# Performance work log

Measured on AMD Instinct MI355X. Metric: run time of the kernel, lower is better.

Reference implementation:

```python
import jax, jax.numpy as jnp
import numpy as np

N, E, G, D = 100000, 400000, 4000, 128
AF, BF, L = 74, 12, 11  # atom/bond feat sizes; L = n_layers-1 GNN layers after GetContext


def _p(k, shape, fan):
    return jax.random.normal(k, shape, dtype=jnp.float32) * (fan ** -0.5)


def setup_inputs() -> dict:
    key = jax.random.key(0)
    ks = iter(jax.random.split(key, 32))
    z = lambda *s: jnp.zeros(s, jnp.float32)
    return dict(
        atom_feats=jax.random.normal(next(ks), (N, AF), jnp.float32),
        bond_feats=jax.random.normal(next(ks), (E, BF), jnp.float32),
        src=jax.random.randint(next(ks), (E,), 0, N, jnp.int32),
        dst=jax.random.randint(next(ks), (E,), 0, N, jnp.int32),
        node_graph_ids=jnp.sort(jax.random.randint(next(ks), (N,), 0, G, jnp.int32)),
        W_node=_p(next(ks), (AF, D), AF), b_node=z(D),
        W_edge1=_p(next(ks), (AF + BF, D), AF + BF), b_edge1=z(D),
        W_edge2=_p(next(ks), (2 * D, 1), 2 * D), b_edge2=z(1),
        W_et=_p(next(ks), (D, D), D), b_et=z(D),
        gru0_Wih=_p(next(ks), (3 * D, D), D), gru0_bih=z(3 * D),
        gru0_Whh=_p(next(ks), (3 * D, D), D), gru0_bhh=z(3 * D),
        Wpe=_p(next(ks), (L, 2 * D, 1), 2 * D), bpe=z(L, 1),
        Wpn=_p(next(ks), (L, D, D), D), bpn=z(L, D),
        gru_Wih=_p(next(ks), (L, 3 * D, D), D), gru_bih=z(L, 3 * D),
        gru_Whh=_p(next(ks), (L, 3 * D, D), D), gru_bhh=z(L, 3 * D),
        Wr1=_p(next(ks), (D, D), D), br1=z(D),
        Wr2=_p(next(ks), (D, D), D), br2=z(D),
    )


def leaky_relu(x):
    return jnp.where(x > 0, x, 0.01 * x)


def edge_softmax(logits, dst):
    # softmax of edge logits grouped by destination node (DGL edge_softmax)
    m = jax.ops.segment_max(logits, dst, num_segments=N)
    m = jnp.where(jnp.isfinite(m), m, 0.0)
    e = jnp.exp(logits - m[dst])
    s = jax.ops.segment_sum(e, dst, num_segments=N)
    return e / s[dst]


def gru_cell(x, h, Wih, bih, Whh, bhh):
    gi = x @ Wih.T + bih
    gh = h @ Whh.T + bhh
    ir, iz, ig = jnp.split(gi, 3, axis=-1)
    hr, hz, hg = jnp.split(gh, 3, axis=-1)
    r = jax.nn.sigmoid(ir + hr)
    z = jax.nn.sigmoid(iz + hz)
    n = jnp.tanh(ig + r * hg)
    return (1.0 - z) * n + z * h


def _attentive_fp(atom_feats, bond_feats, src, dst, node_graph_ids,
                  W_node, b_node, W_edge1, b_edge1, W_edge2, b_edge2,
                  W_et, b_et, gru0_Wih, gru0_bih, gru0_Whh, gru0_bhh,
                  Wpe, bpe, Wpn, bpn, gru_Wih, gru_bih, gru_Whh, gru_bhh,
                  Wr1, br1, Wr2, br2):
    # --- GetContext (dropout = identity at inference) ---
    hv_new = leaky_relu(atom_feats @ W_node + b_node)                       # [N,D]
    he1 = leaky_relu(jnp.concatenate([atom_feats[src], bond_feats], 1) @ W_edge1 + b_edge1)  # [E,D]
    logits = leaky_relu(jnp.concatenate([hv_new[dst], he1], 1) @ W_edge2 + b_edge2)          # [E,1]
    a = edge_softmax(logits, dst)
    c = jax.ops.segment_sum(a * (he1 @ W_et + b_et), dst, num_segments=N)   # [N,D]
    h = jax.nn.relu(gru_cell(jax.nn.elu(c), hv_new, gru0_Wih, gru0_bih, gru0_Whh, gru0_bhh))

    # --- 11 GNNLayers (AttentiveGRU2) via scan over stacked params ---
    def layer(h, p):
        Wpe_l, bpe_l, Wpn_l, bpn_l, Wih, bih, Whh, bhh = p
        lg = leaky_relu(jnp.concatenate([h[dst], h[src]], 1) @ Wpe_l + bpe_l)  # [E,1]
        a = edge_softmax(lg, dst)
        hp = h @ Wpn_l + bpn_l
        c = jax.ops.segment_sum(hp[src] * a, dst, num_segments=N)
        return jax.nn.relu(gru_cell(jax.nn.elu(c), h, Wih, bih, Whh, bhh)), None

    h, _ = jax.lax.scan(layer, h, (Wpe, bpe, Wpn, bpn, gru_Wih, gru_bih, gru_Whh, gru_bhh))

    # --- MLPNodeReadout, mode='mean' ---
    x = jax.nn.relu(h @ Wr1 + br1) @ Wr2 + br2
    sums = jax.ops.segment_sum(x, node_graph_ids, num_segments=G)
    counts = jax.ops.segment_sum(jnp.ones((N, 1), x.dtype), node_graph_ids, num_segments=G)
    return sums / jnp.maximum(counts, 1.0)                                  # [G,D]


def reference(atom_feats, bond_feats, src, dst, node_graph_ids,
              W_node, b_node, W_edge1, b_edge1, W_edge2, b_edge2,
              W_et, b_et, gru0_Wih, gru0_bih, gru0_Whh, gru0_bhh,
              Wpe, bpe, Wpn, bpn, gru_Wih, gru_bih, gru_Whh, gru_bhh,
              Wr1, br1, Wr2, br2):
    return _attentive_fp(atom_feats, bond_feats, src, dst, node_graph_ids,
                         W_node, b_node, W_edge1, b_edge1, W_edge2, b_edge2,
                         W_et, b_et, gru0_Wih, gru0_bih, gru0_Whh, gru0_bhh,
                         Wpe, bpe, Wpn, bpn, gru_Wih, gru_bih, gru_Whh, gru_bhh,
                         Wr1, br1, Wr2, br2)
```

## Files before the change

kernel.cpp:

```cpp
#include <hip/hip_runtime.h>
#include <cstdio>
#include <cstddef>

enum { ACT_NONE = 0, ACT_LEAKY = 1, ACT_RELU = 2 };

typedef __attribute__((ext_vector_type(8))) short short8v;
typedef __attribute__((ext_vector_type(4))) float f32x4;

__device__ __forceinline__ float leakyf(float x) { return x > 0.f ? x : 0.01f * x; }

__device__ __forceinline__ unsigned fenc(float f) {
    unsigned u = __float_as_uint(f);
    return (u & 0x80000000u) ? ~u : (u | 0x80000000u);
}
__device__ __forceinline__ float fdec(unsigned u) {
    return (u & 0x80000000u) ? __uint_as_float(u & 0x7FFFFFFFu) : __uint_as_float(~u);
}

__device__ __forceinline__ unsigned bf16rtn(float x) {
    unsigned u = __float_as_uint(x);
    return (u + 0x7FFFu + ((u >> 16) & 1u)) >> 16;
}
__device__ __forceinline__ void split8(float4 a, float4 b, short8v& hi, short8v& lo) {
    const float v[8] = {a.x, a.y, a.z, a.w, b.x, b.y, b.z, b.w};
#pragma unroll
    for (int i = 0; i < 8; i++) {
        const unsigned hb = bf16rtn(v[i]);
        const float r = v[i] - __uint_as_float(hb << 16);
        hi[i] = (short)hb;
        lo[i] = (short)bf16rtn(r);
    }
}

__global__ __launch_bounds__(256) void wsplit_all_k(
    const float* __restrict__ g0_Wih, const float* __restrict__ g0_Whh,
    const float* __restrict__ gWih,   const float* __restrict__ gWhh,
    const float* __restrict__ Wpn,    const float* __restrict__ W_et,
    const float* __restrict__ Wr1,    const float* __restrict__ Wr2,
    const float* __restrict__ W_e1,   const float* __restrict__ W_node,
    unsigned short* __restrict__ gwHi, unsigned short* __restrict__ gwLo,
    unsigned short* __restrict__ wtHi, unsigned short* __restrict__ wtLo,
    unsigned short* __restrict__ w96Hi, unsigned short* __restrict__ w96Lo)
{
    const int b = blockIdx.x, t = threadIdx.x;
    if (b < 1152) {
        const int slot = b / 96, inner = b % 96;
        const int i4 = (inner * 256 + t) * 4;
        if (i4 >= 98304) return;
        const float* Wih = slot == 0 ? g0_Wih : gWih + (size_t)(slot - 1) * 49152;
        const float* Whh = slot == 0 ? g0_Whh : gWhh + (size_t)(slot - 1) * 49152;
        const float* src = (i4 < 49152) ? (Wih + i4) : (Whh + (i4 - 49152));
        const float4 v = *(const float4*)src;
        const float vv[4] = {v.x, v.y, v.z, v.w};
        unsigned short h4[4], l4[4];
#pragma unroll
        for (int i = 0; i < 4; i++) {
            const unsigned hb = bf16rtn(vv[i]);
            const float r = vv[i] - __uint_as_float(hb << 16);
            h4[i] = (unsigned short)hb;
            l4[i] = (unsigned short)bf16rtn(r);
        }
        *(ushort4*)&gwHi[(size_t)slot * 98304 + i4] = make_ushort4(h4[0], h4[1], h4[2], h4[3]);
        *(ushort4*)&gwLo[(size_t)slot * 98304 + i4] = make_ushort4(l4[0], l4[1], l4[2], l4[3]);
    } else if (b < 2048) {
        const int q = b - 1152;
        const int slot = q / 64, inner = q % 64;
        const int idx = inner * 256 + t;
        if (idx >= 16384) return;
        const float* W = slot < 11 ? Wpn + (size_t)slot * 16384
                        : slot == 11 ? W_et : slot == 12 ? Wr1 : Wr2;
        const int k = idx >> 7, col = idx & 127;
        const float v = W[idx];
        const unsigned hb = bf16rtn(v);
        const float r = v - __uint_as_float(hb << 16);
        wtHi[(size_t)slot * 16384 + col * 128 + k] = (unsigned short)hb;
        wtLo[(size_t)slot * 16384 + col * 128 + k] = (unsigned short)bf16rtn(r);
    } else {
        const int q = b - 2048;
        const int slot = q / 48, inner = q % 48;
        const int idx = inner * 256 + t;
        if (idx >= 12288) return;
        const float* W = slot == 0 ? W_e1 : W_node;
        const int K   = slot == 0 ? 86 : 74;
        const int col = idx / 96, k = idx - col * 96;
        const float v = (k < K) ? W[(size_t)k * 128 + col] : 0.f;
        const unsigned hb = bf16rtn(v);
        const float r = v - __uint_as_float(hb << 16);
        w96Hi[(size_t)slot * 12288 + idx] = (unsigned short)hb;
        w96Lo[(size_t)slot * 12288 + idx] = (unsigned short)bf16rtn(r);
    }
}

__global__ __launch_bounds__(512) void gru_fused_mfma_k(
    const float* __restrict__ cbuf, const unsigned short* __restrict__ whi,
    const unsigned short* __restrict__ wlo, const float* __restrict__ bih,
    const float* __restrict__ bhh, float* __restrict__ h,
    const float* __restrict__ wa, const float* __restrict__ wb,
    float* __restrict__ pd, float* __restrict__ ps,
    const unsigned short* __restrict__ w3hi, const unsigned short* __restrict__ w3lo,
    const float* __restrict__ b3, float* __restrict__ out3, int act3, int M)
{
    __shared__ __align__(16) char smem[64 * 132 * 4];
    short (*lhi)[4][64][8] = (short(*)[4][64][8])smem;
    short (*llo)[4][64][8] = (short(*)[4][64][8])(smem + 16384);
    float (*fbuf)[132] = (float(*)[132])smem;

    const int t    = threadIdx.x;
    const int lane = t & 63;
    const int w    = t >> 6;
    const int rBase = blockIdx.x * 64;

    const int sRS = t >> 3, sQ = t & 7;
    const int sRow = rBase + sRS;
    const int sRT = sRS >> 4, sLrow = sRS & 15;

    auto stage = [&](const float* __restrict__ A, bool doElu) {
#pragma unroll
        for (int half = 0; half < 2; half++) {
            const int k0 = sQ * 16 + half * 8;
            const int kc = k0 >> 5;
            const int g  = (k0 & 31) >> 3;
            float4 f0 = make_float4(0.f, 0.f, 0.f, 0.f);
            float4 f1 = make_float4(0.f, 0.f, 0.f, 0.f);
            if (sRow < M) {
                f0 = *(const float4*)&A[(size_t)sRow * 128 + k0];
                f1 = *(const float4*)&A[(size_t)sRow * 128 + k0 + 4];
                if (doElu) {
                    f0.x = f0.x > 0.f ? f0.x : expm1f(f0.x);
                    f0.y = f0.y > 0.f ? f0.y : expm1f(f0.y);
                    f0.z = f0.z > 0.f ? f0.z : expm1f(f0.z);
                    f0.w = f0.w > 0.f ? f0.w : expm1f(f0.w);
                    f1.x = f1.x > 0.f ? f1.x : expm1f(f1.x);
                    f1.y = f1.y > 0.f ? f1.y : expm1f(f1.y);
                    f1.z = f1.z > 0.f ? f1.z : expm1f(f1.z);
                    f1.w = f1.w > 0.f ? f1.w : expm1f(f1.w);
                }
            }
            short8v h8, l8;
            split8(f0, f1, h8, l8);
            *(short8v*)&lhi[sRT][kc][sLrow + g * 16][0] = h8;
            *(short8v*)&llo[sRT][kc][sLrow + g * 16][0] = l8;
        }
    };

    f32x4 accr[4], accz[4], accig[4], acchg[4];
#pragma unroll
    for (int rt = 0; rt < 4; rt++) {
        accr[rt]  = (f32x4){0.f, 0.f, 0.f, 0.f};
        accz[rt]  = (f32x4){0.f, 0.f, 0.f, 0.f};
        accig[rt] = (f32x4){0.f, 0.f, 0.f, 0.f};
        acchg[rt] = (f32x4){0.f, 0.f, 0.f, 0.f};
    }

    const int cw   = w * 16 + (lane & 15);
    const int koff = (lane >> 4) * 8;

    stage(cbuf, true);
    __syncthreads();
#pragma unroll
    for (int kc = 0; kc < 4; kc++) {
        short8v bh[3], bl[3];
#pragma unroll
        for (int g = 0; g < 3; g++) {
            const size_t off = (size_t)(g * 128 + cw) * 128 + kc * 32 + koff;
            bh[g] = *(const short8v*)&whi[off];
            bl[g] = *(const short8v*)&wlo[off];
        }
#pragma unroll
        for (int rt = 0; rt < 4; rt++) {
            const short8v ah = *(const short8v*)&lhi[rt][kc][lane][0];
            const short8v al = *(const short8v*)&llo[rt][kc][lane][0];
            accr[rt]  = __builtin_amdgcn_mfma_f32_16x16x32_bf16(ah, bh[0], accr[rt], 0, 0, 0);
            accr[rt]  = __builtin_amdgcn_mfma_f32_16x16x32_bf16(al, bh[0], accr[rt], 0, 0, 0);
            accr[rt]  = __builtin_amdgcn_mfma_f32_16x16x32_bf16(ah, bl[0], accr[rt], 0, 0, 0);
            accz[rt]  = __builtin_amdgcn_mfma_f32_16x16x32_bf16(ah, bh[1], accz[rt], 0, 0, 0);
            accz[rt]  = __builtin_amdgcn_mfma_f32_16x16x32_bf16(al, bh[1], accz[rt], 0, 0, 0);
            accz[rt]  = __builtin_amdgcn_mfma_f32_16x16x32_bf16(ah, bl[1], accz[rt], 0, 0, 0);
            accig[rt] = __builtin_amdgcn_mfma_f32_16x16x32_bf16(ah, bh[2], accig[rt], 0, 0, 0);
            accig[rt] = __builtin_amdgcn_mfma_f32_16x16x32_bf16(al, bh[2], accig[rt], 0, 0, 0);
            accig[rt] = __builtin_amdgcn_mfma_f32_16x16x32_bf16(ah, bl[2], accig[rt], 0, 0, 0);
        }
    }
    __syncthreads();

    stage(h, false);
    __syncthreads();
#pragma unroll
    for (int kc = 0; kc < 4; kc++) {
        short8v bh[3], bl[3];
#pragma unroll
        for (int g = 0; g < 3; g++) {
            const size_t off = (size_t)(384 + g * 128 + cw) * 128 + kc * 32 + koff;
            bh[g] = *(const short8v*)&whi[off];
            bl[g] = *(const short8v*)&wlo[off];
        }
#pragma unroll
        for (int rt = 0; rt < 4; rt++) {
            const short8v ah = *(const short8v*)&lhi[rt][kc][lane][0];
            const short8v al = *(const short8v*)&llo[rt][kc][lane][0];
            accr[rt]  = __builtin_amdgcn_mfma_f32_16x16x32_bf16(ah, bh[0], accr[rt], 0, 0, 0);
            accr[rt]  = __builtin_amdgcn_mfma_f32_16x16x32_bf16(al, bh[0], accr[rt], 0, 0, 0);
            accr[rt]  = __builtin_amdgcn_mfma_f32_16x16x32_bf16(ah, bl[0], accr[rt], 0, 0, 0);
            accz[rt]  = __builtin_amdgcn_mfma_f32_16x16x32_bf16(ah, bh[1], accz[rt], 0, 0, 0);
            accz[rt]  = __builtin_amdgcn_mfma_f32_16x16x32_bf16(al, bh[1], accz[rt], 0, 0, 0);
            accz[rt]  = __builtin_amdgcn_mfma_f32_16x16x32_bf16(ah, bl[1], accz[rt], 0, 0, 0);
            acchg[rt] = __builtin_amdgcn_mfma_f32_16x16x32_bf16(ah, bh[2], acchg[rt], 0, 0, 0);
            acchg[rt] = __builtin_amdgcn_mfma_f32_16x16x32_bf16(al, bh[2], acchg[rt], 0, 0, 0);
            acchg[rt] = __builtin_amdgcn_mfma_f32_16x16x32_bf16(ah, bl[2], acchg[rt], 0, 0, 0);
        }
    }

    const bool post = (wa != nullptr) || (w3hi != nullptr);
    const float br_  = bih[cw] + bhh[cw];
    const float bz_  = bih[128 + cw] + bhh[128 + cw];
    const float big_ = bih[256 + cw];
    const float bhg_ = bhh[256 + cw];
    if (post) __syncthreads();
#pragma unroll
    for (int rt = 0; rt < 4; rt++) {
        const int lr0 = rt * 16 + ((lane >> 4) << 2);
#pragma unroll
        for (int i = 0; i < 4; i++) {
            const int row = rBase + lr0 + i;
            const bool ok = (row < M);
            float hnew = 0.f;
            if (ok) {
                const float hv = h[(size_t)row * 128 + cw];
                const float r  = 1.f / (1.f + expf(-(accr[rt][i] + br_)));
                const float z  = 1.f / (1.f + expf(-(accz[rt][i] + bz_)));
                const float nn = tanhf(accig[rt][i] + big_ + r * (acchg[rt][i] + bhg_));
                hnew = fmaxf((1.f - z) * nn + z * hv, 0.f);
                h[(size_t)row * 128 + cw] = hnew;
            }
            if (post) fbuf[lr0 + i][cw] = hnew;
        }
    }
    if (!post) return;
    __syncthreads();

    if (wa && t < 64 && rBase + t < M) {
        float accd = 0.f, accs = 0.f;
        for (int cc = 0; cc < 128; cc++) {
            const float hv = fbuf[t][cc];
            accd = fmaf(hv, wa[cc], accd);
            accs = fmaf(hv, wb[cc], accs);
        }
        pd[rBase + t] = accd;
        ps[rBase + t] = accs;
    }

    if (w3hi) {
        float4 rv[2][2];
#pragma unroll
        for (int half = 0; half < 2; half++) {
            const int k0 = sQ * 16 + half * 8;
            rv[half][0] = *(const float4*)&fbuf[sRS][k0];
            rv[half][1] = *(const float4*)&fbuf[sRS][k0 + 4];
        }
        __syncthreads();
#pragma unroll
        for (int half = 0; half < 2; half++) {
            const int k0 = sQ * 16 + half * 8;
            const int kc = k0 >> 5;
            const int g  = (k0 & 31) >> 3;
            short8v h8, l8;
            split8(rv[half][0], rv[half][1], h8, l8);
            *(short8v*)&lhi[sRT][kc][sLrow + g * 16][0] = h8;
            *(short8v*)&llo[sRT][kc][sLrow + g * 16][0] = l8;
        }
        __syncthreads();

        f32x4 acc3[4];
#pragma unroll
        for (int rt = 0; rt < 4; rt++) acc3[rt] = (f32x4){0.f, 0.f, 0.f, 0.f};
#pragma unroll
        for (int kc = 0; kc < 4; kc++) {
            const size_t off = (size_t)cw * 128 + kc * 32 + koff;
            const short8v bh = *(const short8v*)&w3hi[off];
            const short8v bl = *(const short8v*)&w3lo[off];
#pragma unroll
            for (int rt = 0; rt < 4; rt++) {
                const short8v ah = *(const short8v*)&lhi[rt][kc][lane][0];
                const short8v al = *(const short8v*)&llo[rt][kc][lane][0];
                acc3[rt] = __builtin_amdgcn_mfma_f32_16x16x32_bf16(ah, bh, acc3[rt], 0, 0, 0);
                acc3[rt] = __builtin_amdgcn_mfma_f32_16x16x32_bf16(al, bh, acc3[rt], 0, 0, 0);
                acc3[rt] = __builtin_amdgcn_mfma_f32_16x16x32_bf16(ah, bl, acc3[rt], 0, 0, 0);
            }
        }
        const float b0 = b3[cw];
#pragma unroll
        for (int rt = 0; rt < 4; rt++) {
            const int r0 = rBase + rt * 16 + ((lane >> 4) << 2);
#pragma unroll
            for (int i = 0; i < 4; i++) {
                const int row = r0 + i;
                if (row >= M) continue;
                float v = acc3[rt][i] + b0;
                if (act3 == ACT_LEAKY)      v = v > 0.f ? v : 0.01f * v;
                else if (act3 == ACT_RELU)  v = fmaxf(v, 0.f);
                out3[(size_t)row * 128 + cw] = v;
            }
        }
    }
}

__global__ __launch_bounds__(512) void mfma128_k(
    const float* __restrict__ A, const unsigned short* __restrict__ whi,
    const unsigned short* __restrict__ wlo, const float* __restrict__ bias,
    float* __restrict__ C, int M, int actOut)
{
    __shared__ short lhi[4][4][64][8];
    __shared__ short llo[4][4][64][8];
    const int t    = threadIdx.x;
    const int lane = t & 63;
    const int w    = t >> 6;
    const int rBase = blockIdx.x * 64;

    {
        const int rS = t >> 3, q = t & 7;
        const int row = rBase + rS;
        const int rt = rS >> 4, lrow = rS & 15;
#pragma unroll
        for (int half = 0; half < 2; half++) {
            const int k0 = q * 16 + half * 8;
            const int kc = k0 >> 5;
            const int g  = (k0 & 31) >> 3;
            float4 f0 = make_float4(0.f, 0.f, 0.f, 0.f);
            float4 f1 = make_float4(0.f, 0.f, 0.f, 0.f);
            if (row < M) {
                f0 = *(const float4*)&A[(size_t)row * 128 + k0];
                f1 = *(const float4*)&A[(size_t)row * 128 + k0 + 4];
            }
            short8v h8, l8;
            split8(f0, f1, h8, l8);
            *(short8v*)&lhi[rt][kc][lrow + g * 16][0] = h8;
            *(short8v*)&llo[rt][kc][lrow + g * 16][0] = l8;
        }
    }
    __syncthreads();

    f32x4 acc[4];
#pragma unroll
    for (int rt = 0; rt < 4; rt++) acc[rt] = (f32x4){0.f, 0.f, 0.f, 0.f};

    const int cw   = w * 16 + (lane & 15);
    const int koff = (lane >> 4) * 8;

#pragma unroll
    for (int kc = 0; kc < 4; kc++) {
        const size_t off = (size_t)cw * 128 + kc * 32 + koff;
        const short8v bh = *(const short8v*)&whi[off];
        const short8v bl = *(const short8v*)&wlo[off];
#pragma unroll
        for (int rt = 0; rt < 4; rt++) {
            const short8v ah = *(const short8v*)&lhi[rt][kc][lane][0];
            const short8v al = *(const short8v*)&llo[rt][kc][lane][0];
            acc[rt] = __builtin_amdgcn_mfma_f32_16x16x32_bf16(ah, bh, acc[rt], 0, 0, 0);
            acc[rt] = __builtin_amdgcn_mfma_f32_16x16x32_bf16(al, bh, acc[rt], 0, 0, 0);
            acc[rt] = __builtin_amdgcn_mfma_f32_16x16x32_bf16(ah, bl, acc[rt], 0, 0, 0);
        }
    }

    const float b0 = bias[cw];
#pragma unroll
    for (int rt = 0; rt < 4; rt++) {
        const int r0 = rBase + rt * 16 + ((lane >> 4) << 2);
#pragma unroll
        for (int i = 0; i < 4; i++) {
            const int row = r0 + i;
            if (row >= M) continue;
            float v = acc[rt][i] + b0;
            if (actOut == ACT_LEAKY)      v = v > 0.f ? v : 0.01f * v;
            else if (actOut == ACT_RELU)  v = fmaxf(v, 0.f);
            C[(size_t)row * 128 + cw] = v;
        }
    }
}

__global__ __launch_bounds__(512) void mfma96_k(
    const float* __restrict__ A1, const float* __restrict__ A2,
    const int* __restrict__ idx,
    const unsigned short* __restrict__ whi, const unsigned short* __restrict__ wlo,
    const float* __restrict__ bias, float* __restrict__ C,
    const float* __restrict__ dotW, float* __restrict__ dotOut,
    const float* __restrict__ ee, const float* __restrict__ sd,
    const int* __restrict__ dstI, float* __restrict__ cAtom,
    int writeC, int M, int K1, int actOut)
{
    __shared__ __align__(16) char smem[64 * 130 * 4];
    short (*lhi)[3][64][8] = (short(*)[3][64][8])smem;
    short (*llo)[3][64][8] = (short(*)[3][64][8])(smem + 12288);
    float (*fbuf)[130] = (float(*)[130])smem;

    const int t    = threadIdx.x;
    const int lane = t & 63;
    const int w    = t >> 6;
    const int rBase = blockIdx.x * 64;

    {
        const int rS = t >> 3, q = t & 7;
        const int row = rBase + rS;
        const int rt = rS >> 4, lrow = rS & 15;
#pragma unroll
        for (int half = 0; half < 2; half++) {
            const int k0 = q * 16 + half * 8;
            if (k0 >= 96) continue;
            const int kc = k0 >> 5;
            const int g  = (k0 & 31) >> 3;
            float v[8] = {0.f, 0.f, 0.f, 0.f, 0.f, 0.f, 0.f, 0.f};
            if (row < M) {
                const int ar = idx ? idx[row] : row;
                const float* __restrict__ a1 = A1 + (size_t)ar * K1;
#pragma unroll
                for (int j = 0; j < 8; j++) {
                    const int k = k0 + j;
                    if (k < K1)                 v[j] = a1[k];
                    else if (A2 && k < K1 + 12) v[j] = A2[(size_t)row * 12 + (k - K1)];
                }
            }
            short8v h8, l8;
            split8(make_float4(v[0], v[1], v[2], v[3]),
                   make_float4(v[4], v[5], v[6], v[7]), h8, l8);
            *(short8v*)&lhi[rt][kc][lrow + g * 16][0] = h8;
            *(short8v*)&llo[rt][kc][lrow + g * 16][0] = l8;
        }
    }
    __syncthreads();

    f32x4 acc[4];
#pragma unroll
    for (int rt = 0; rt < 4; rt++) acc[rt] = (f32x4){0.f, 0.f, 0.f, 0.f};

    const int cw   = w * 16 + (lane & 15);
    const int koff = (lane >> 4) * 8;

#pragma unroll
    for (int kc = 0; kc < 3; kc++) {
        const size_t off = (size_t)cw * 96 + kc * 32 + koff;
        const short8v bh = *(const short8v*)&whi[off];
        const short8v bl = *(const short8v*)&wlo[off];
#pragma unroll
        for (int rt = 0; rt < 4; rt++) {
            const short8v ah = *(const short8v*)&lhi[rt][kc][lane][0];
            const short8v al = *(const short8v*)&llo[rt][kc][lane][0];
            acc[rt] = __builtin_amdgcn_mfma_f32_16x16x32_bf16(ah, bh, acc[rt], 0, 0, 0);
            acc[rt] = __builtin_amdgcn_mfma_f32_16x16x32_bf16(al, bh, acc[rt], 0, 0, 0);
            acc[rt] = __builtin_amdgcn_mfma_f32_16x16x32_bf16(ah, bl, acc[rt], 0, 0, 0);
        }
    }

    const float b0 = bias[cw];
    if (dotOut) __syncthreads();
#pragma unroll
    for (int rt = 0; rt < 4; rt++) {
        const int lr0 = rt * 16 + ((lane >> 4) << 2);
#pragma unroll
        for (int i = 0; i < 4; i++) {
            const int row = rBase + lr0 + i;
            const bool ok = (row < M);
            float v = acc[rt][i] + b0;
            if (actOut == ACT_LEAKY)      v = v > 0.f ? v : 0.01f * v;
            else if (actOut == ACT_RELU)  v = fmaxf(v, 0.f);
            if (ok && writeC) C[(size_t)row * 128 + cw] = v;
            if (ok && ee) {
                const int d = dstI[row];
                const float a = ee[row] / sd[d];
                atomicAdd(&cAtom[(size_t)d * 128 + cw], a * v);
            }
            if (dotOut) fbuf[lr0 + i][cw] = ok ? v : 0.f;
        }
    }
    if (dotOut) {
        __syncthreads();
        if (t < 64 && rBase + t < M) {
            float accd = 0.f;
            for (int cc = 0; cc < 128; cc++)
                accd = fmaf(fbuf[t][cc], dotW[cc], accd);
            dotOut[rBase + t] = accd;
        }
    }
}

__global__ __launch_bounds__(256) void edge_lgc_k(
    const float* __restrict__ pd, const float* __restrict__ pe,
    const float* __restrict__ b2, const int* __restrict__ dst,
    float* __restrict__ lg, unsigned* __restrict__ m_u, int E)
{
    const int e = blockIdx.x * blockDim.x + threadIdx.x;
    if (e >= E) return;
    const int d = dst[e];
    const float v = leakyf(pd[d] + pe[e] + b2[0]);
    lg[e] = v;
    atomicMax(&m_u[d], fenc(v));
}

__global__ __launch_bounds__(256) void edge_exp_k(
    float* __restrict__ lg, const unsigned* __restrict__ m_u,
    float* __restrict__ s, const int* __restrict__ dst, int E)
{
    const int e = blockIdx.x * blockDim.x + threadIdx.x;
    if (e >= E) return;
    const int d = dst[e];
    const float ex = expf(lg[e] - fdec(m_u[d]));
    lg[e] = ex;
    atomicAdd(&s[d], ex);
}

__global__ __launch_bounds__(256) void hist_k(
    const int* __restrict__ dst, unsigned* __restrict__ cnt, int E)
{
    const int e = blockIdx.x * blockDim.x + threadIdx.x;
    if (e < E) atomicAdd(&cnt[dst[e]], 1u);
}

__global__ __launch_bounds__(1024) void scan_k(
    const unsigned* __restrict__ cnt, int* __restrict__ rp, int N)
{
    __shared__ int wsum[16];
    __shared__ int carry;
    const int t = threadIdx.x, lane = t & 63, wid = t >> 6;
    if (t == 0) carry = 0;
    __syncthreads();
    for (int base = 0; base < N; base += 1024) {
        const int i = base + t;
        const int v = (i < N) ? (int)cnt[i] : 0;
        int x = v;
#pragma unroll
        for (int o = 1; o < 64; o <<= 1) {
            const int y = __shfl_up(x, o, 64);
            if (lane >= o) x += y;
        }
        if (lane == 63) wsum[wid] = x;
        __syncthreads();
        if (wid == 0) {
            const int wv = (lane < 16) ? wsum[lane] : 0;
            int wx = wv;
#pragma unroll
            for (int o = 1; o < 16; o <<= 1) {
                const int y = __shfl_up(wx, o, 64);
                if (lane >= o) wx += y;
            }
            if (lane < 16) wsum[lane] = wx - wv;
        }
        __syncthreads();
        const int excl = carry + wsum[wid] + x - v;
        if (i < N) rp[i] = excl;
        __syncthreads();
        if (t == 1023) carry = excl + v;
        __syncthreads();
    }
    if (t == 0) rp[N] = carry;
}

__global__ __launch_bounds__(256) void fill_csr_k(
    const int* __restrict__ dst, int* __restrict__ pos,
    int* __restrict__ eidx, int E)
{
    const int e = blockIdx.x * blockDim.x + threadIdx.x;
    if (e < E) {
        const int p = atomicAdd(&pos[dst[e]], 1);
        eidx[p] = e;
    }
}

__global__ __launch_bounds__(256) void layer_gather_k(
    const int* __restrict__ rp, const int* __restrict__ eidx,
    const int* __restrict__ src,
    const float* __restrict__ pd, const float* __restrict__ ps,
    const float* __restrict__ bpe,
    const float* __restrict__ hp, float* __restrict__ c, int N)
{
    const int d = blockIdx.x * 4 + (threadIdx.x >> 6);
    const int l = threadIdx.x & 63;
    if (d >= N) return;
    const int beg = rp[d], end = rp[d + 1];
    float acc0 = 0.f, acc1 = 0.f;
    if (beg < end) {
        const float pdd = pd[d];
        const float b   = bpe[0];
        float m = -3.4e38f;
        for (int e = beg + l; e < end; e += 64)
            m = fmaxf(m, leakyf(pdd + ps[src[eidx[e]]] + b));
#pragma unroll
        for (int o = 32; o; o >>= 1) m = fmaxf(m, __shfl_xor(m, o, 64));
        float s = 0.f;
        for (int e = beg + l; e < end; e += 64)
            s += expf(leakyf(pdd + ps[src[eidx[e]]] + b) - m);
#pragma unroll
        for (int o = 32; o; o >>= 1) s += __shfl_xor(s, o, 64);
        const float inv = 1.f / s;
        for (int e = beg; e < end; ++e) {
            const int sr = src[eidx[e]];
            const float a = expf(leakyf(pdd + ps[sr] + b) - m) * inv;
            const float2 v = *(const float2*)&hp[(size_t)sr * 128 + l * 2];
            acc0 = fmaf(a, v.x, acc0);
            acc1 = fmaf(a, v.y, acc1);
        }
    }
    *(float2*)&c[(size_t)d * 128 + l * 2] = make_float2(acc0, acc1);
}

__global__ __launch_bounds__(256) void readout_mean_k(
    const float* __restrict__ x, const int* __restrict__ grp,
    float* __restrict__ out, int G)
{
    const int g = blockIdx.x * 4 + (threadIdx.x >> 6);
    const int l = threadIdx.x & 63;
    if (g >= G) return;
    const int beg = grp[g], end = grp[g + 1];
    float s0 = 0.f, s1 = 0.f;
    for (int r = beg; r < end; ++r) {
        const float2 v = *(const float2*)&x[(size_t)r * 128 + l * 2];
        s0 += v.x;
        s1 += v.y;
    }
    const float inv = 1.f / fmaxf((float)(end - beg), 1.f);
    *(float2*)&out[(size_t)g * 128 + l * 2] = make_float2(s0 * inv, s1 * inv);
}

extern "C" void kernel_launch(void* const* d_in, const int* in_sizes, int n_in,
                              void* d_out, int out_size, void* d_ws, size_t ws_size,
                              hipStream_t stream)
{
    const float* atom   = (const float*)d_in[0];
    const float* bond   = (const float*)d_in[1];
    const int*   src    = (const int*)d_in[2];
    const int*   dst    = (const int*)d_in[3];
    const int*   ngid   = (const int*)d_in[4];
    const float* W_node = (const float*)d_in[5];
    const float* b_node = (const float*)d_in[6];
    const float* W_e1   = (const float*)d_in[7];
    const float* b_e1   = (const float*)d_in[8];
    const float* W_e2   = (const float*)d_in[9];
    const float* b_e2   = (const float*)d_in[10];
    const float* W_et   = (const float*)d_in[11];
    const float* b_et   = (const float*)d_in[12];
    const float* g0_Wih = (const float*)d_in[13];
    const float* g0_bih = (const float*)d_in[14];
    const float* g0_Whh = (const float*)d_in[15];
    const float* g0_bhh = (const float*)d_in[16];
    const float* Wpe    = (const float*)d_in[17];
    const float* bpe    = (const float*)d_in[18];
    const float* Wpn    = (const float*)d_in[19];
    const float* bpn    = (const float*)d_in[20];
    const float* gWih   = (const float*)d_in[21];
    const float* gbih   = (const float*)d_in[22];
    const float* gWhh   = (const float*)d_in[23];
    const float* gbhh   = (const float*)d_in[24];
    const float* Wr1    = (const float*)d_in[25];
    const float* br1    = (const float*)d_in[26];
    const float* Wr2    = (const float*)d_in[27];
    const float* br2    = (const float*)d_in[28];

    const int N = in_sizes[0] / 74;
    const int E = in_sizes[1] / 12;
    const int G = out_size / 128;
    const int L = in_sizes[18];

    char* w = (char*)d_ws;
    auto align256 = [](size_t b) { return (b + 255) & ~(size_t)255; };
    auto alloc = [&](size_t bytes) {
        void* p = (void*)w;
        w += align256(bytes);
        return p;
    };
    float*    h    = (float*)alloc((size_t)N * 128 * 4);
    float*    c    = (float*)alloc((size_t)N * 128 * 4);
    float*    hp   = (float*)alloc((size_t)N * 128 * 4);
    int*      rp   = (int*)alloc((size_t)(N + 1) * 4);
    int*      posb = (int*)alloc((size_t)N * 4);
    int*      eidx = (int*)alloc((size_t)E * 4);
    int*      grp  = (int*)alloc((size_t)(G + 1) * 4);
    unsigned short* gwHi  = (unsigned short*)alloc((size_t)12 * 98304 * 2);
    unsigned short* gwLo  = (unsigned short*)alloc((size_t)12 * 98304 * 2);
    unsigned short* wtHi  = (unsigned short*)alloc((size_t)14 * 16384 * 2);
    unsigned short* wtLo  = (unsigned short*)alloc((size_t)14 * 16384 * 2);
    unsigned short* w96Hi = (unsigned short*)alloc((size_t)2 * 12288 * 2);
    unsigned short* w96Lo = (unsigned short*)alloc((size_t)2 * 12288 * 2);
    float*    pd   = (float*)alloc((size_t)N * 4);
    float*    ps   = (float*)alloc((size_t)N * 4);
    unsigned* m_u  = (unsigned*)alloc((size_t)N * 4);
    float*    sden = (float*)alloc((size_t)N * 4);
    float*    pe   = (float*)alloc((size_t)E * 4);
    float*    lg   = (float*)alloc((size_t)E * 4);
    if ((size_t)(w - (char*)d_ws) > ws_size) {
        fprintf(stderr, "kernel_launch: ws too small: need %zu, have %zu\n",
                (size_t)(w - (char*)d_ws), ws_size);
        return;
    }
    float* out = (float*)d_out;

    const dim3 blk(256);
    auto g64 = [](int M) { return dim3((unsigned)((M + 63) / 64)); };
    const dim3 gEdge((unsigned)((E + 255) / 256));

    wsplit_all_k<<<dim3(2144), blk, 0, stream>>>(
        g0_Wih, g0_Whh, gWih, gWhh, Wpn, W_et, Wr1, Wr2, W_e1, W_node,
        gwHi, gwLo, wtHi, wtLo, w96Hi, w96Lo);

    auto run_gru = [&](int slot, const float* bih, const float* bhh,
                       const float* wav, const float* wbv,
                       int w3slot, const float* b3, float* out3, int act3) {
        gru_fused_mfma_k<<<g64(N), dim3(512), 0, stream>>>(
            c, gwHi + (size_t)slot * 98304, gwLo + (size_t)slot * 98304,
            bih, bhh, h, wav, wbv, pd, ps,
            wtHi + (size_t)w3slot * 16384, wtLo + (size_t)w3slot * 16384,
            b3, out3, act3, N);
    };
    auto run_mfma128 = [&](const float* A, int slot, const float* bias,
                           float* C, int act) {
        mfma128_k<<<g64(N), dim3(512), 0, stream>>>(
            A, wtHi + (size_t)slot * 16384, wtLo + (size_t)slot * 16384, bias, C, N, act);
    };

    hipMemsetAsync(m_u, 0, (size_t)N * 4, stream);
    hist_k<<<gEdge, blk, 0, stream>>>(dst, m_u, E);
    scan_k<<<dim3(1), dim3(1024), 0, stream>>>(m_u, rp, N);
    hipMemcpyAsync(posb, rp, (size_t)N * 4, hipMemcpyDeviceToDevice, stream);
    fill_csr_k<<<gEdge, blk, 0, stream>>>(dst, posb, eidx, E);
    hipMemsetAsync(m_u, 0, (size_t)G * 4, stream);
    hist_k<<<dim3((unsigned)((N + 255) / 256)), blk, 0, stream>>>(ngid, m_u, N);
    scan_k<<<dim3(1), dim3(1024), 0, stream>>>(m_u, grp, G);

    mfma96_k<<<g64(N), dim3(512), 0, stream>>>(
        atom, nullptr, nullptr, w96Hi + 12288, w96Lo + 12288, b_node, h,
        W_e2, pd, nullptr, nullptr, nullptr, nullptr, 1, N, 74, ACT_LEAKY);
    mfma96_k<<<g64(E), dim3(512), 0, stream>>>(
        atom, bond, src, w96Hi, w96Lo, b_e1,
        nullptr, W_e2 + 128, pe, nullptr, nullptr, nullptr, nullptr, 0, E, 74, ACT_LEAKY);
    hipMemsetAsync(m_u, 0, (size_t)N * 4, stream);
    hipMemsetAsync(sden, 0, (size_t)N * 4, stream);
    edge_lgc_k<<<gEdge, blk, 0, stream>>>(pd, pe, b_e2, dst, lg, m_u, E);
    edge_exp_k<<<gEdge, blk, 0, stream>>>(lg, m_u, sden, dst, E);
    hipMemsetAsync(c, 0, (size_t)N * 128 * 4, stream);
    mfma96_k<<<g64(E), dim3(512), 0, stream>>>(
        atom, bond, src, w96Hi, w96Lo, b_e1,
        nullptr, nullptr, nullptr, lg, sden, dst, c, 0, E, 74, ACT_LEAKY);
    run_mfma128(c, 11, b_et, c, ACT_NONE);
    run_gru(0, g0_bih, g0_bhh, Wpe, Wpe + 128, 0, bpn, hp, ACT_NONE);

    for (int l = 0; l < L; ++l) {
        layer_gather_k<<<dim3((unsigned)((N + 3) / 4)), blk, 0, stream>>>(
            rp, eidx, src, pd, ps, bpe + l, hp, c, N);
        const bool more = (l + 1 < L);
        if (more) {
            run_gru(l + 1, gbih + (size_t)l * 384, gbhh + (size_t)l * 384,
                    Wpe + (size_t)(l + 1) * 256, Wpe + (size_t)(l + 1) * 256 + 128,
                    l + 1, bpn + (size_t)(l + 1) * 128, hp, ACT_NONE);
        } else {
            run_gru(l + 1, gbih + (size_t)l * 384, gbhh + (size_t)l * 384,
                    nullptr, nullptr, 12, br1, c, ACT_RELU);
        }
    }

    run_mfma128(c, 13, br2, hp, ACT_NONE);
    readout_mean_k<<<dim3((unsigned)((G + 3) / 4)), blk, 0, stream>>>(hp, grp, out, G);

    (void)n_in;
}
```

Baseline: 3.505 ms.

## Fuse per-layer attention gather into GRU kernel and sort edges by destination

```diff
diff --git a/kernel.cpp b/kernel.cpp
--- a/kernel.cpp
+++ b/kernel.cpp
@@ -31,6 +31,7 @@
         lo[i] = (short)bf16rtn(r);
     }
 }
+__device__ __forceinline__ float eluf(float x) { return x > 0.f ? x : expm1f(x); }
 
 __global__ __launch_bounds__(256) void wsplit_all_k(
     const float* __restrict__ g0_Wih, const float* __restrict__ g0_Whh,
@@ -98,7 +99,10 @@
     const float* __restrict__ wa, const float* __restrict__ wb,
     float* __restrict__ pd, float* __restrict__ ps,
     const unsigned short* __restrict__ w3hi, const unsigned short* __restrict__ w3lo,
-    const float* __restrict__ b3, float* __restrict__ out3, int act3, int M)
+    const float* __restrict__ b3, float* __restrict__ out3, int act3,
+    const int* __restrict__ grp_rp, const int* __restrict__ gsrc,
+    const float* __restrict__ ghp, const float* __restrict__ gbpe,
+    const float* __restrict__ pdIn, const float* __restrict__ psIn, int M)
 {
     __shared__ __align__(16) char smem[64 * 132 * 4];
     short (*lhi)[4][64][8] = (short(*)[4][64][8])smem;
@@ -126,14 +130,8 @@
                 f0 = *(const float4*)&A[(size_t)sRow * 128 + k0];
                 f1 = *(const float4*)&A[(size_t)sRow * 128 + k0 + 4];
                 if (doElu) {
-                    f0.x = f0.x > 0.f ? f0.x : expm1f(f0.x);
-                    f0.y = f0.y > 0.f ? f0.y : expm1f(f0.y);
-                    f0.z = f0.z > 0.f ? f0.z : expm1f(f0.z);
-                    f0.w = f0.w > 0.f ? f0.w : expm1f(f0.w);
-                    f1.x = f1.x > 0.f ? f1.x : expm1f(f1.x);
-                    f1.y = f1.y > 0.f ? f1.y : expm1f(f1.y);
-                    f1.z = f1.z > 0.f ? f1.z : expm1f(f1.z);
-                    f1.w = f1.w > 0.f ? f1.w : expm1f(f1.w);
+                    f0.x = eluf(f0.x); f0.y = eluf(f0.y); f0.z = eluf(f0.z); f0.w = eluf(f0.w);
+                    f1.x = eluf(f1.x); f1.y = eluf(f1.y); f1.z = eluf(f1.z); f1.w = eluf(f1.w);
                 }
             }
             short8v h8, l8;
@@ -155,8 +153,67 @@
     const int cw   = w * 16 + (lane & 15);
     const int koff = (lane >> 4) * 8;
 
-    stage(cbuf, true);
+    if (grp_rp) {
+        const float b = gbpe[0];
+#pragma unroll
+        for (int j = 0; j < 8; j++) {
+            const int lrow = w * 8 + j;
+            const int d = rBase + lrow;
+            float acc0 = 0.f, acc1 = 0.f;
+            if (d < M) {
+                const int beg = grp_rp[d], end = grp_rp[d + 1];
+                if (beg < end) {
+                    const float pdd = pdIn[d];
+                    float m = -3.4e38f;
+                    for (int e = beg + lane; e < end; e += 64)
+                        m = fmaxf(m, leakyf(pdd + psIn[gsrc[e]] + b));
+#pragma unroll
+                    for (int o = 32; o; o >>= 1) m = fmaxf(m, __shfl_xor(m, o, 64));
+                    float s = 0.f;
+                    for (int e = beg + lane; e < end; e += 64)
+                        s += expf(leakyf(pdd + psIn[gsrc[e]] + b) - m);
+#pragma unroll
+                    for (int o = 32; o; o >>= 1) s += __shfl_xor(s, o, 64);
+                    const float inv = 1.f / s;
+                    for (int e = beg; e < end; ++e) {
+                        const int sr = gsrc[e];
+                        const float a = expf(leakyf(pdd + psIn[sr] + b) - m) * inv;
+                        const float2 v = *(const float2*)&ghp[(size_t)sr * 128 + lane * 2];
+                        acc0 = fmaf(a, v.x, acc0);
+                        acc1 = fmaf(a, v.y, acc1);
+                    }
+                }
+            }
+            fbuf[lrow][lane * 2]     = acc0;
+            fbuf[lrow][lane * 2 + 1] = acc1;
+        }
+        __syncthreads();
+        float4 rv[2][2];
+#pragma unroll
+        for (int half = 0; half < 2; half++) {
+            const int k0 = sQ * 16 + half * 8;
+            rv[half][0] = *(const float4*)&fbuf[sRS][k0];
+            rv[half][1] = *(const float4*)&fbuf[sRS][k0 + 4];
+        }
+        __syncthreads();
+#pragma unroll
+        for (int half = 0; half < 2; half++) {
+            const int k0 = sQ * 16 + half * 8;
+            const int kc = k0 >> 5;
+            const int g  = (k0 & 31) >> 3;
+            float4 f0 = rv[half][0], f1 = rv[half][1];
+            f0.x = eluf(f0.x); f0.y = eluf(f0.y); f0.z = eluf(f0.z); f0.w = eluf(f0.w);
+            f1.x = eluf(f1.x); f1.y = eluf(f1.y); f1.z = eluf(f1.z); f1.w = eluf(f1.w);
+            short8v h8, l8;
+            split8(f0, f1, h8, l8);
+            *(short8v*)&lhi[sRT][kc][sLrow + g * 16][0] = h8;
+            *(short8v*)&llo[sRT][kc][sLrow + g * 16][0] = l8;
+        }
+    } else {
+        stage(cbuf, true);
+    }
     __syncthreads();
+
 #pragma unroll
     for (int kc = 0; kc < 4; kc++) {
         short8v bh[3], bl[3];
@@ -379,7 +436,7 @@
 
 __global__ __launch_bounds__(512) void mfma96_k(
     const float* __restrict__ A1, const float* __restrict__ A2,
-    const int* __restrict__ idx,
+    const int* __restrict__ idx, const int* __restrict__ idx2,
     const unsigned short* __restrict__ whi, const unsigned short* __restrict__ wlo,
     const float* __restrict__ bias, float* __restrict__ C,
     const float* __restrict__ dotW, float* __restrict__ dotOut,
@@ -409,13 +466,14 @@
             const int g  = (k0 & 31) >> 3;
             float v[8] = {0.f, 0.f, 0.f, 0.f, 0.f, 0.f, 0.f, 0.f};
             if (row < M) {
-                const int ar = idx ? idx[row] : row;
+                const int ar  = idx ? idx[row] : row;
+                const int ar2 = idx2 ? idx2[row] : row;
                 const float* __restrict__ a1 = A1 + (size_t)ar * K1;
 #pragma unroll
                 for (int j = 0; j < 8; j++) {
                     const int k = k0 + j;
                     if (k < K1)                 v[j] = a1[k];
-                    else if (A2 && k < K1 + 12) v[j] = A2[(size_t)row * 12 + (k - K1)];
+                    else if (A2 && k < K1 + 12) v[j] = A2[(size_t)ar2 * 12 + (k - K1)];
                 }
             }
             short8v h8, l8;
@@ -450,7 +508,8 @@
     }
 
     const float b0 = bias[cw];
-    if (dotOut) __syncthreads();
+    const bool useF = (dotOut != nullptr) || (ee != nullptr);
+    if (useF) __syncthreads();
 #pragma unroll
     for (int rt = 0; rt < 4; rt++) {
         const int lr0 = rt * 16 + ((lane >> 4) << 2);
@@ -462,15 +521,37 @@
             if (actOut == ACT_LEAKY)      v = v > 0.f ? v : 0.01f * v;
             else if (actOut == ACT_RELU)  v = fmaxf(v, 0.f);
             if (ok && writeC) C[(size_t)row * 128 + cw] = v;
-            if (ok && ee) {
-                const int d = dstI[row];
-                const float a = ee[row] / sd[d];
-                atomicAdd(&cAtom[(size_t)d * 128 + cw], a * v);
-            }
-            if (dotOut) fbuf[lr0 + i][cw] = ok ? v : 0.f;
-        }
-    }
-    if (dotOut) {
+            if (ee) {
+                float av = 0.f;
+                if (ok) {
+                    const int eo = idx2 ? idx2[row] : row;
+                    av = ee[eo] / sd[dstI[row]] * v;
+                }
+                fbuf[lr0 + i][cw] = av;
+            } else if (dotOut) {
+                fbuf[lr0 + i][cw] = ok ? v : 0.f;
+            }
+        }
+    }
+    if (ee) {
+        __syncthreads();
+        const int col = t & 127;
+        const int r0  = (t >> 7) * 16;
+        float acc2 = 0.f;
+        int cur = -1;
+        for (int j = 0; j < 16; j++) {
+            const int row = rBase + r0 + j;
+            if (row >= M) break;
+            const int d = dstI[row];
+            if (d != cur) {
+                if (cur >= 0) atomicAdd(&cAtom[(size_t)cur * 128 + col], acc2);
+                cur = d;
+                acc2 = 0.f;
+            }
+            acc2 += fbuf[r0 + j][col];
+        }
+        if (cur >= 0) atomicAdd(&cAtom[(size_t)cur * 128 + col], acc2);
+    } else if (dotOut) {
         __syncthreads();
         if (t < 64 && rBase + t < M) {
             float accd = 0.f;
@@ -553,51 +634,18 @@
 }
 
 __global__ __launch_bounds__(256) void fill_csr_k(
-    const int* __restrict__ dst, int* __restrict__ pos,
-    int* __restrict__ eidx, int E)
+    const int* __restrict__ dst, const int* __restrict__ src,
+    int* __restrict__ pos, int* __restrict__ eidx,
+    int* __restrict__ srcS, int* __restrict__ dstS, int E)
 {
     const int e = blockIdx.x * blockDim.x + threadIdx.x;
     if (e < E) {
-        const int p = atomicAdd(&pos[dst[e]], 1);
+        const int d = dst[e];
+        const int p = atomicAdd(&pos[d], 1);
         eidx[p] = e;
-    }
-}
-
-__global__ __launch_bounds__(256) void layer_gather_k(
-    const int* __restrict__ rp, const int* __restrict__ eidx,
-    const int* __restrict__ src,
-    const float* __restrict__ pd, const float* __restrict__ ps,
-    const float* __restrict__ bpe,
-    const float* __restrict__ hp, float* __restrict__ c, int N)
-{
-    const int d = blockIdx.x * 4 + (threadIdx.x >> 6);
-    const int l = threadIdx.x & 63;
-    if (d >= N) return;
-    const int beg = rp[d], end = rp[d + 1];
-    float acc0 = 0.f, acc1 = 0.f;
-    if (beg < end) {
-        const float pdd = pd[d];
-        const float b   = bpe[0];
-        float m = -3.4e38f;
-        for (int e = beg + l; e < end; e += 64)
-            m = fmaxf(m, leakyf(pdd + ps[src[eidx[e]]] + b));
-#pragma unroll
-        for (int o = 32; o; o >>= 1) m = fmaxf(m, __shfl_xor(m, o, 64));
-        float s = 0.f;
-        for (int e = beg + l; e < end; e += 64)
-            s += expf(leakyf(pdd + ps[src[eidx[e]]] + b) - m);
-#pragma unroll
-        for (int o = 32; o; o >>= 1) s += __shfl_xor(s, o, 64);
-        const float inv = 1.f / s;
-        for (int e = beg; e < end; ++e) {
-            const int sr = src[eidx[e]];
-            const float a = expf(leakyf(pdd + ps[sr] + b) - m) * inv;
-            const float2 v = *(const float2*)&hp[(size_t)sr * 128 + l * 2];
-            acc0 = fmaf(a, v.x, acc0);
-            acc1 = fmaf(a, v.y, acc1);
-        }
-    }
-    *(float2*)&c[(size_t)d * 128 + l * 2] = make_float2(acc0, acc1);
+        srcS[p] = src[e];
+        dstS[p] = d;
+    }
 }
 
 __global__ __launch_bounds__(256) void readout_mean_k(
@@ -666,10 +714,13 @@
     };
     float*    h    = (float*)alloc((size_t)N * 128 * 4);
     float*    c    = (float*)alloc((size_t)N * 128 * 4);
-    float*    hp   = (float*)alloc((size_t)N * 128 * 4);
+    float*    hpA  = (float*)alloc((size_t)N * 128 * 4);
+    float*    hpB  = (float*)alloc((size_t)N * 128 * 4);
     int*      rp   = (int*)alloc((size_t)(N + 1) * 4);
     int*      posb = (int*)alloc((size_t)N * 4);
     int*      eidx = (int*)alloc((size_t)E * 4);
+    int*      srcS = (int*)alloc((size_t)E * 4);
+    int*      dstS = (int*)alloc((size_t)E * 4);
     int*      grp  = (int*)alloc((size_t)(G + 1) * 4);
     unsigned short* gwHi  = (unsigned short*)alloc((size_t)12 * 98304 * 2);
     unsigned short* gwLo  = (unsigned short*)alloc((size_t)12 * 98304 * 2);
@@ -677,8 +728,10 @@
     unsigned short* wtLo  = (unsigned short*)alloc((size_t)14 * 16384 * 2);
     unsigned short* w96Hi = (unsigned short*)alloc((size_t)2 * 12288 * 2);
     unsigned short* w96Lo = (unsigned short*)alloc((size_t)2 * 12288 * 2);
-    float*    pd   = (float*)alloc((size_t)N * 4);
-    float*    ps   = (float*)alloc((size_t)N * 4);
+    float*    pdA  = (float*)alloc((size_t)N * 4);
+    float*    psA  = (float*)alloc((size_t)N * 4);
+    float*    pdB  = (float*)alloc((size_t)N * 4);
+    float*    psB  = (float*)alloc((size_t)N * 4);
     unsigned* m_u  = (unsigned*)alloc((size_t)N * 4);
     float*    sden = (float*)alloc((size_t)N * 4);
     float*    pe   = (float*)alloc((size_t)E * 4);
@@ -700,12 +753,16 @@
 
     auto run_gru = [&](int slot, const float* bih, const float* bhh,
                        const float* wav, const float* wbv,
-                       int w3slot, const float* b3, float* out3, int act3) {
+                       float* pdW, float* psW,
+                       int w3slot, const float* b3, float* out3, int act3,
+                       const float* gBpe, const float* hpR,
+                       const float* pdR, const float* psR) {
         gru_fused_mfma_k<<<g64(N), dim3(512), 0, stream>>>(
             c, gwHi + (size_t)slot * 98304, gwLo + (size_t)slot * 98304,
-            bih, bhh, h, wav, wbv, pd, ps,
+            bih, bhh, h, wav, wbv, pdW, psW,
             wtHi + (size_t)w3slot * 16384, wtLo + (size_t)w3slot * 16384,
-            b3, out3, act3, N);
+            b3, out3, act3,
+            gBpe ? rp : nullptr, srcS, hpR, gBpe, pdR, psR, N);
     };
     auto run_mfma128 = [&](const float* A, int slot, const float* bias,
                            float* C, int act) {
@@ -717,44 +774,53 @@
     hist_k<<<gEdge, blk, 0, stream>>>(dst, m_u, E);
     scan_k<<<dim3(1), dim3(1024), 0, stream>>>(m_u, rp, N);
     hipMemcpyAsync(posb, rp, (size_t)N * 4, hipMemcpyDeviceToDevice, stream);
-    fill_csr_k<<<gEdge, blk, 0, stream>>>(dst, posb, eidx, E);
+    fill_csr_k<<<gEdge, blk, 0, stream>>>(dst, src, posb, eidx, srcS, dstS, E);
     hipMemsetAsync(m_u, 0, (size_t)G * 4, stream);
     hist_k<<<dim3((unsigned)((N + 255) / 256)), blk, 0, stream>>>(ngid, m_u, N);
     scan_k<<<dim3(1), dim3(1024), 0, stream>>>(m_u, grp, G);
 
     mfma96_k<<<g64(N), dim3(512), 0, stream>>>(
-        atom, nullptr, nullptr, w96Hi + 12288, w96Lo + 12288, b_node, h,
-        W_e2, pd, nullptr, nullptr, nullptr, nullptr, 1, N, 74, ACT_LEAKY);
+        atom, nullptr, nullptr, nullptr, w96Hi + 12288, w96Lo + 12288, b_node, h,
+        W_e2, pdA, nullptr, nullptr, nullptr, nullptr, 1, N, 74, ACT_LEAKY);
     mfma96_k<<<g64(E), dim3(512), 0, stream>>>(
-        atom, bond, src, w96Hi, w96Lo, b_e1,
+        atom, bond, src, nullptr, w96Hi, w96Lo, b_e1,
         nullptr, W_e2 + 128, pe, nullptr, nullptr, nullptr, nullptr, 0, E, 74, ACT_LEAKY);
     hipMemsetAsync(m_u, 0, (size_t)N * 4, stream);
     hipMemsetAsync(sden, 0, (size_t)N * 4, stream);
-    edge_lgc_k<<<gEdge, blk, 0, stream>>>(pd, pe, b_e2, dst, lg, m_u, E);
+    edge_lgc_k<<<gEdge, blk, 0, stream>>>(pdA, pe, b_e2, dst, lg, m_u, E);
     edge_exp_k<<<gEdge, blk, 0, stream>>>(lg, m_u, sden, dst, E);
     hipMemsetAsync(c, 0, (size_t)N * 128 * 4, stream);
     mfma96_k<<<g64(E), dim3(512), 0, stream>>>(
-        atom, bond, src, w96Hi, w96Lo, b_e1,
-        nullptr, nullptr, nullptr, lg, sden, dst, c, 0, E, 74, ACT_LEAKY);
+        atom, bond, srcS, eidx, w96Hi, w96Lo, b_e1,
+        nullptr, nullptr, nullptr, lg, sden, dstS, c, 0, E, 74, ACT_LEAKY);
     run_mfma128(c, 11, b_et, c, ACT_NONE);
-    run_gru(0, g0_bih, g0_bhh, Wpe, Wpe + 128, 0, bpn, hp, ACT_NONE);
+    run_gru(0, g0_bih, g0_bhh, Wpe, Wpe + 128, pdA, psA,
+            0, bpn, hpA, ACT_NONE, nullptr, nullptr, nullptr, nullptr);
 
     for (int l = 0; l < L; ++l) {
-        layer_gather_k<<<dim3((unsigned)((N + 3) / 4)), blk, 0, stream>>>(
-            rp, eidx, src, pd, ps, bpe + l, hp, c, N);
         const bool more = (l + 1 < L);
+        const float* pdR = (l % 2 == 0) ? pdA : pdB;
+        const float* psR = (l % 2 == 0) ? psA : psB;
+        float* pdW = (l % 2 == 0) ? pdB : pdA;
+        float* psW = (l % 2 == 0) ? psB : psA;
+        const float* hpR = (l % 2 == 0) ? hpA : hpB;
+        float*       hpW = (l % 2 == 0) ? hpB : hpA;
         if (more) {
             run_gru(l + 1, gbih + (size_t)l * 384, gbhh + (size_t)l * 384,
                     Wpe + (size_t)(l + 1) * 256, Wpe + (size_t)(l + 1) * 256 + 128,
-                    l + 1, bpn + (size_t)(l + 1) * 128, hp, ACT_NONE);
+                    pdW, psW,
+                    l + 1, bpn + (size_t)(l + 1) * 128, hpW, ACT_NONE,
+                    bpe + l, hpR, pdR, psR);
         } else {
             run_gru(l + 1, gbih + (size_t)l * 384, gbhh + (size_t)l * 384,
-                    nullptr, nullptr, 12, br1, c, ACT_RELU);
-        }
-    }
-
-    run_mfma128(c, 13, br2, hp, ACT_NONE);
-    readout_mean_k<<<dim3((unsigned)((G + 3) / 4)), blk, 0, stream>>>(hp, grp, out, G);
+                    nullptr, nullptr, nullptr, nullptr,
+                    12, br1, c, ACT_RELU,
+                    bpe + l, hpR, pdR, psR);
+        }
+    }
+
+    run_mfma128(c, 13, br2, hpA, ACT_NONE);
+    readout_mean_k<<<dim3((unsigned)((G + 3) / 4)), blk, 0, stream>>>(hpA, grp, out, G);
 
     (void)n_in;
 }
```

Result: slower. 5.358 ms (+52.9%).

## Process edges in dst-sorted order and pre-reduce scatter atomics per block

Applied to the files above, without the earlier changes.

```diff
diff --git a/kernel.cpp b/kernel.cpp
--- a/kernel.cpp
+++ b/kernel.cpp
@@ -31,6 +31,7 @@
         lo[i] = (short)bf16rtn(r);
     }
 }
+__device__ __forceinline__ float eluf(float x) { return x > 0.f ? x : expm1f(x); }
 
 __global__ __launch_bounds__(256) void wsplit_all_k(
     const float* __restrict__ g0_Wih, const float* __restrict__ g0_Whh,
@@ -126,14 +127,8 @@
                 f0 = *(const float4*)&A[(size_t)sRow * 128 + k0];
                 f1 = *(const float4*)&A[(size_t)sRow * 128 + k0 + 4];
                 if (doElu) {
-                    f0.x = f0.x > 0.f ? f0.x : expm1f(f0.x);
-                    f0.y = f0.y > 0.f ? f0.y : expm1f(f0.y);
-                    f0.z = f0.z > 0.f ? f0.z : expm1f(f0.z);
-                    f0.w = f0.w > 0.f ? f0.w : expm1f(f0.w);
-                    f1.x = f1.x > 0.f ? f1.x : expm1f(f1.x);
-                    f1.y = f1.y > 0.f ? f1.y : expm1f(f1.y);
-                    f1.z = f1.z > 0.f ? f1.z : expm1f(f1.z);
-                    f1.w = f1.w > 0.f ? f1.w : expm1f(f1.w);
+                    f0.x = eluf(f0.x); f0.y = eluf(f0.y); f0.z = eluf(f0.z); f0.w = eluf(f0.w);
+                    f1.x = eluf(f1.x); f1.y = eluf(f1.y); f1.z = eluf(f1.z); f1.w = eluf(f1.w);
                 }
             }
             short8v h8, l8;
@@ -379,7 +374,7 @@
 
 __global__ __launch_bounds__(512) void mfma96_k(
     const float* __restrict__ A1, const float* __restrict__ A2,
-    const int* __restrict__ idx,
+    const int* __restrict__ idx, const int* __restrict__ idx2,
     const unsigned short* __restrict__ whi, const unsigned short* __restrict__ wlo,
     const float* __restrict__ bias, float* __restrict__ C,
     const float* __restrict__ dotW, float* __restrict__ dotOut,
@@ -409,13 +404,14 @@
             const int g  = (k0 & 31) >> 3;
             float v[8] = {0.f, 0.f, 0.f, 0.f, 0.f, 0.f, 0.f, 0.f};
             if (row < M) {
-                const int ar = idx ? idx[row] : row;
+                const int ar  = idx ? idx[row] : row;
+                const int ar2 = idx2 ? idx2[row] : row;
                 const float* __restrict__ a1 = A1 + (size_t)ar * K1;
 #pragma unroll
                 for (int j = 0; j < 8; j++) {
                     const int k = k0 + j;
                     if (k < K1)                 v[j] = a1[k];
-                    else if (A2 && k < K1 + 12) v[j] = A2[(size_t)row * 12 + (k - K1)];
+                    else if (A2 && k < K1 + 12) v[j] = A2[(size_t)ar2 * 12 + (k - K1)];
                 }
             }
             short8v h8, l8;
@@ -450,7 +446,8 @@
     }
 
     const float b0 = bias[cw];
-    if (dotOut) __syncthreads();
+    const bool useF = (dotOut != nullptr) || (ee != nullptr);
+    if (useF) __syncthreads();
 #pragma unroll
     for (int rt = 0; rt < 4; rt++) {
         const int lr0 = rt * 16 + ((lane >> 4) << 2);
@@ -462,15 +459,37 @@
             if (actOut == ACT_LEAKY)      v = v > 0.f ? v : 0.01f * v;
             else if (actOut == ACT_RELU)  v = fmaxf(v, 0.f);
             if (ok && writeC) C[(size_t)row * 128 + cw] = v;
-            if (ok && ee) {
-                const int d = dstI[row];
-                const float a = ee[row] / sd[d];
-                atomicAdd(&cAtom[(size_t)d * 128 + cw], a * v);
-            }
-            if (dotOut) fbuf[lr0 + i][cw] = ok ? v : 0.f;
-        }
-    }
-    if (dotOut) {
+            if (ee) {
+                float av = 0.f;
+                if (ok) {
+                    const int eo = idx2 ? idx2[row] : row;
+                    av = ee[eo] / sd[dstI[row]] * v;
+                }
+                fbuf[lr0 + i][cw] = av;
+            } else if (dotOut) {
+                fbuf[lr0 + i][cw] = ok ? v : 0.f;
+            }
+        }
+    }
+    if (ee) {
+        __syncthreads();
+        const int col = t & 127;
+        const int r0  = (t >> 7) * 16;
+        float acc2 = 0.f;
+        int cur = -1;
+        for (int j = 0; j < 16; j++) {
+            const int row = rBase + r0 + j;
+            if (row >= M) break;
+            const int d = dstI[row];
+            if (d != cur) {
+                if (cur >= 0) atomicAdd(&cAtom[(size_t)cur * 128 + col], acc2);
+                cur = d;
+                acc2 = 0.f;
+            }
+            acc2 += fbuf[r0 + j][col];
+        }
+        if (cur >= 0) atomicAdd(&cAtom[(size_t)cur * 128 + col], acc2);
+    } else if (dotOut) {
         __syncthreads();
         if (t < 64 && rBase + t < M) {
             float accd = 0.f;
@@ -553,19 +572,22 @@
 }
 
 __global__ __launch_bounds__(256) void fill_csr_k(
-    const int* __restrict__ dst, int* __restrict__ pos,
-    int* __restrict__ eidx, int E)
+    const int* __restrict__ dst, const int* __restrict__ src,
+    int* __restrict__ pos, int* __restrict__ eidx,
+    int* __restrict__ srcS, int* __restrict__ dstS, int E)
 {
     const int e = blockIdx.x * blockDim.x + threadIdx.x;
     if (e < E) {
-        const int p = atomicAdd(&pos[dst[e]], 1);
+        const int d = dst[e];
+        const int p = atomicAdd(&pos[d], 1);
         eidx[p] = e;
+        srcS[p] = src[e];
+        dstS[p] = d;
     }
 }
 
 __global__ __launch_bounds__(256) void layer_gather_k(
-    const int* __restrict__ rp, const int* __restrict__ eidx,
-    const int* __restrict__ src,
+    const int* __restrict__ rp, const int* __restrict__ srcS,
     const float* __restrict__ pd, const float* __restrict__ ps,
     const float* __restrict__ bpe,
     const float* __restrict__ hp, float* __restrict__ c, int N)
@@ -580,17 +602,17 @@
         const float b   = bpe[0];
         float m = -3.4e38f;
         for (int e = beg + l; e < end; e += 64)
-            m = fmaxf(m, leakyf(pdd + ps[src[eidx[e]]] + b));
+            m = fmaxf(m, leakyf(pdd + ps[srcS[e]] + b));
 #pragma unroll
         for (int o = 32; o; o >>= 1) m = fmaxf(m, __shfl_xor(m, o, 64));
         float s = 0.f;
         for (int e = beg + l; e < end; e += 64)
-            s += expf(leakyf(pdd + ps[src[eidx[e]]] + b) - m);
+            s += expf(leakyf(pdd + ps[srcS[e]] + b) - m);
 #pragma unroll
         for (int o = 32; o; o >>= 1) s += __shfl_xor(s, o, 64);
         const float inv = 1.f / s;
         for (int e = beg; e < end; ++e) {
-            const int sr = src[eidx[e]];
+            const int sr = srcS[e];
             const float a = expf(leakyf(pdd + ps[sr] + b) - m) * inv;
             const float2 v = *(const float2*)&hp[(size_t)sr * 128 + l * 2];
             acc0 = fmaf(a, v.x, acc0);
@@ -670,6 +692,8 @@
     int*      rp   = (int*)alloc((size_t)(N + 1) * 4);
     int*      posb = (int*)alloc((size_t)N * 4);
     int*      eidx = (int*)alloc((size_t)E * 4);
+    int*      srcS = (int*)alloc((size_t)E * 4);
+    int*      dstS = (int*)alloc((size_t)E * 4);
     int*      grp  = (int*)alloc((size_t)(G + 1) * 4);
     unsigned short* gwHi  = (unsigned short*)alloc((size_t)12 * 98304 * 2);
     unsigned short* gwLo  = (unsigned short*)alloc((size_t)12 * 98304 * 2);
@@ -717,16 +741,16 @@
     hist_k<<<gEdge, blk, 0, stream>>>(dst, m_u, E);
     scan_k<<<dim3(1), dim3(1024), 0, stream>>>(m_u, rp, N);
     hipMemcpyAsync(posb, rp, (size_t)N * 4, hipMemcpyDeviceToDevice, stream);
-    fill_csr_k<<<gEdge, blk, 0, stream>>>(dst, posb, eidx, E);
+    fill_csr_k<<<gEdge, blk, 0, stream>>>(dst, src, posb, eidx, srcS, dstS, E);
     hipMemsetAsync(m_u, 0, (size_t)G * 4, stream);
     hist_k<<<dim3((unsigned)((N + 255) / 256)), blk, 0, stream>>>(ngid, m_u, N);
     scan_k<<<dim3(1), dim3(1024), 0, stream>>>(m_u, grp, G);
 
     mfma96_k<<<g64(N), dim3(512), 0, stream>>>(
-        atom, nullptr, nullptr, w96Hi + 12288, w96Lo + 12288, b_node, h,
+        atom, nullptr, nullptr, nullptr, w96Hi + 12288, w96Lo + 12288, b_node, h,
         W_e2, pd, nullptr, nullptr, nullptr, nullptr, 1, N, 74, ACT_LEAKY);
     mfma96_k<<<g64(E), dim3(512), 0, stream>>>(
-        atom, bond, src, w96Hi, w96Lo, b_e1,
+        atom, bond, src, nullptr, w96Hi, w96Lo, b_e1,
         nullptr, W_e2 + 128, pe, nullptr, nullptr, nullptr, nullptr, 0, E, 74, ACT_LEAKY);
     hipMemsetAsync(m_u, 0, (size_t)N * 4, stream);
     hipMemsetAsync(sden, 0, (size_t)N * 4, stream);
@@ -734,14 +758,14 @@
     edge_exp_k<<<gEdge, blk, 0, stream>>>(lg, m_u, sden, dst, E);
     hipMemsetAsync(c, 0, (size_t)N * 128 * 4, stream);
     mfma96_k<<<g64(E), dim3(512), 0, stream>>>(
-        atom, bond, src, w96Hi, w96Lo, b_e1,
-        nullptr, nullptr, nullptr, lg, sden, dst, c, 0, E, 74, ACT_LEAKY);
+        atom, bond, srcS, eidx, w96Hi, w96Lo, b_e1,
+        nullptr, nullptr, nullptr, lg, sden, dstS, c, 0, E, 74, ACT_LEAKY);
     run_mfma128(c, 11, b_et, c, ACT_NONE);
     run_gru(0, g0_bih, g0_bhh, Wpe, Wpe + 128, 0, bpn, hp, ACT_NONE);
 
     for (int l = 0; l < L; ++l) {
         layer_gather_k<<<dim3((unsigned)((N + 3) / 4)), blk, 0, stream>>>(
-            rp, eidx, src, pd, ps, bpe + l, hp, c, N);
+            rp, srcS, pd, ps, bpe + l, hp, c, N);
         const bool more = (l + 1 < L);
         if (more) {
             run_gru(l + 1, gbih + (size_t)l * 384, gbhh + (size_t)l * 384,
```

Result: faster. 3.325 ms (-5.1%).
